# Performance work log

Hardware: AMD Instinct MI355X
Metric: run time of the kernel (lower is better)

Reference implementation:

```python
import jax, jax.numpy as jnp
import numpy as np

B, S, H = 4, 256, 768
NUM_BASIC = 4
NUM_REL = 32            # labels 1..31 are real edges, 0 = no edge
NUM_ALL = 2 * NUM_REL   # bidir: forward slots 0..31, reverse slots 33..63


def setup_inputs() -> dict:
    key = jax.random.key(0)
    k1, k2, k3, k4, k5 = jax.random.split(key, 5)
    hidden_states = jax.random.normal(k1, (B, S, H), dtype=jnp.float32)
    rels = jax.random.randint(k2, (B, S, S), 0, NUM_REL, dtype=jnp.int32)
    # xavier-ish init scale for params
    basic_matrix = jax.random.normal(k3, (NUM_BASIC, H, H), dtype=jnp.float32) * 0.02
    rel_weight = jax.random.normal(k4, (NUM_ALL, NUM_BASIC), dtype=jnp.float32) * 0.1
    self_weight = jax.random.normal(k5, (H, H), dtype=jnp.float32) * 0.02  # Linear weight (out,in)
    return {"hidden_states": hidden_states, "rels": rels,
            "basic_matrix": basic_matrix, "rel_weight": rel_weight,
            "self_weight": self_weight}


def reference(hidden_states, rels, basic_matrix, rel_weight, self_weight):
    dt = hidden_states.dtype
    # forward-direction one-hot relation tensor [B, NUM_ALL, S, S], masked where rels == 0
    fwd_mask = (rels > 0).astype(dt)                                   # [B,S,S]
    fwd_oh = jax.nn.one_hot(rels, NUM_ALL, axis=1, dtype=dt) * fwd_mask[:, None]
    # reverse direction (bidir): labels shifted by NUM_REL, zeroed where no edge
    rev_rels_raw = jnp.transpose(rels, (0, 2, 1))
    rev_rels = jnp.where(rev_rels_raw > 0, rev_rels_raw + NUM_REL, 0)  # {0} U {33..63}
    rev_mask = (rev_rels > 0).astype(dt)
    rev_oh = jax.nn.one_hot(rev_rels, NUM_ALL, axis=1, dtype=dt) * rev_mask[:, None]
    rel_tensor = fwd_oh + rev_oh                                       # [B,R,S,S]

    # basis decomposition: per-relation transform [R, H, H]
    rel_matrix = jnp.einsum('rb,bio->rio', rel_weight, basic_matrix)
    # per-relation transformed hidden states [B,R,S,H]
    r_hidden = jnp.einsum('bsi,rio->brso', hidden_states, rel_matrix)
    # adjacency aggregation [B,R,S,H]
    r_ctx = jnp.einsum('brij,brjo->brio', rel_tensor, r_hidden)
    # mean over neighbors (clamp count at 1)
    num_neighbors = jnp.maximum(rel_tensor.sum(-1), 1.0)               # [B,R,S]
    r_ctx = r_ctx / num_neighbors[..., None]
    context = r_ctx.sum(axis=1)                                        # [B,S,H]
    self_layer = hidden_states @ self_weight.T
    return self_layer + context
```

## Files before the change

### kernel.cpp

```cpp
#include <hip/hip_runtime.h>
#include <stdint.h>

typedef unsigned short u16;
typedef unsigned int u32;
typedef __attribute__((ext_vector_type(8))) short short8;
typedef __attribute__((ext_vector_type(4))) float float4v;

#define Bb 4
#define Ss 256
#define Hh 768
#define NALL 64


__device__ __forceinline__ float b2f(u16 h) {
    u32 u = ((u32)h) << 16;
    float f;
    __builtin_memcpy(&f, &u, 4);
    return f;
}
__device__ __forceinline__ u16 f2b(float f) {
    u32 u;
    __builtin_memcpy(&u, &f, 4);
    u = (u + 0x7fffu + ((u >> 16) & 1u)) >> 16;
    return (u16)u;
}
union pk8 { uint4 v; u16 e[8]; };
__device__ __forceinline__ uint4 cvt8(float4 f0, float4 f1) {
    pk8 r;
    r.e[0] = f2b(f0.x); r.e[1] = f2b(f0.y); r.e[2] = f2b(f0.z); r.e[3] = f2b(f0.w);
    r.e[4] = f2b(f1.x); r.e[5] = f2b(f1.y); r.e[6] = f2b(f1.z); r.e[7] = f2b(f1.w);
    return r.v;
}

__device__ __forceinline__ void gemm_tile(const float* __restrict__ aB,
                                          const float* __restrict__ bB,
                                          int niter, u16* As, u16* Bs,
                                          float4v* acc, int t) {
    const int row = t >> 2, kk = (t & 3) * 16;
    const int w = t >> 6, l = t & 63, quad = l >> 4, l16 = l & 15;
#pragma unroll
    for (int c = 0; c < 4; ++c) acc[c] = (float4v){0.f, 0.f, 0.f, 0.f};
    float4 a0 = *(const float4*)aB, a1 = *(const float4*)(aB + 4);
    float4 a2 = *(const float4*)(aB + 8), a3 = *(const float4*)(aB + 12);
    float4 b0 = *(const float4*)bB, b1 = *(const float4*)(bB + 4);
    float4 b2 = *(const float4*)(bB + 8), b3 = *(const float4*)(bB + 12);
    for (int s = 0; s < niter; ++s) {
        __syncthreads();
        *(uint4*)(&As[row * 72 + kk]) = cvt8(a0, a1);
        *(uint4*)(&As[row * 72 + kk + 8]) = cvt8(a2, a3);
        *(uint4*)(&Bs[row * 72 + kk]) = cvt8(b0, b1);
        *(uint4*)(&Bs[row * 72 + kk + 8]) = cvt8(b2, b3);
        __syncthreads();
        if (s + 1 < niter) {
            const float* ap = aB + (s + 1) * 64;
            const float* bp = bB + (s + 1) * 64;
            a0 = *(const float4*)ap; a1 = *(const float4*)(ap + 4);
            a2 = *(const float4*)(ap + 8); a3 = *(const float4*)(ap + 12);
            b0 = *(const float4*)bp; b1 = *(const float4*)(bp + 4);
            b2 = *(const float4*)(bp + 8); b3 = *(const float4*)(bp + 12);
        }
#pragma unroll
        for (int k2 = 0; k2 < 64; k2 += 32) {
            const short8 af = *(const short8*)(&As[(16 * w + l16) * 72 + k2 + quad * 8]);
#pragma unroll
            for (int c = 0; c < 4; ++c) {
                const short8 bfr = *(const short8*)(&Bs[(16 * c + l16) * 72 + k2 + quad * 8]);
                acc[c] = __builtin_amdgcn_mfma_f32_16x16x32_bf16(af, bfr, acc[c], 0, 0, 0);
            }
        }
    }
}

__global__ __launch_bounds__(256, 4) void k_phase1(const float* __restrict__ h,
                                                   const int* __restrict__ rels,
                                                   const float* __restrict__ basic,
                                                   const float* __restrict__ relw,
                                                   const float* __restrict__ selfw,
                                                   u16* __restrict__ coefC,
                                                   u16* __restrict__ Gt,
                                                   u16* __restrict__ S) {
    __shared__ __align__(16) u16 As[64 * 72];
    __shared__ __align__(16) u16 Bs[64 * 72];
    const int t = threadIdx.x;
    const int z = blockIdx.x;
    const int row = t >> 2, kk = (t & 3) * 16;
    const int w = t >> 6, l = t & 63, quad = l >> 4, l16 = l & 15;

    if (z < 768) {
        const int ot = z % 12, jt = (z / 12) % 4, bk = z / 48;
        const int b = bk >> 2, q = bk & 3;
        const float* aB = h + ((size_t)b * Ss + jt * 64 + row) * Hh + kk;
        const float* bp = basic + ((size_t)q * Hh + row) * Hh + ot * 64 + kk;

        float4v acc[4];
#pragma unroll
        for (int c = 0; c < 4; ++c) acc[c] = (float4v){0.f, 0.f, 0.f, 0.f};
        float4 a0 = *(const float4*)aB, a1 = *(const float4*)(aB + 4);
        float4 a2 = *(const float4*)(aB + 8), a3 = *(const float4*)(aB + 12);
        float4 b0 = *(const float4*)bp, b1 = *(const float4*)(bp + 4);
        float4 b2 = *(const float4*)(bp + 8), b3 = *(const float4*)(bp + 12);

        for (int s = 0; s < 12; ++s) {
            __syncthreads();
            *(uint4*)(&As[row * 72 + kk]) = cvt8(a0, a1);
            *(uint4*)(&As[row * 72 + kk + 8]) = cvt8(a2, a3);
            {
                pk8 t0, t1;
                t0.v = cvt8(b0, b1);
                t1.v = cvt8(b2, b3);
#pragma unroll
                for (int m = 0; m < 8; ++m) Bs[(kk + m) * 72 + row] = t0.e[m];
#pragma unroll
                for (int m = 0; m < 8; ++m) Bs[(kk + 8 + m) * 72 + row] = t1.e[m];
            }
            __syncthreads();
            if (s + 1 < 12) {
                const float* ap = aB + (s + 1) * 64;
                const float* bq = bp + (size_t)(s + 1) * 64 * Hh;
                a0 = *(const float4*)ap; a1 = *(const float4*)(ap + 4);
                a2 = *(const float4*)(ap + 8); a3 = *(const float4*)(ap + 12);
                b0 = *(const float4*)bq; b1 = *(const float4*)(bq + 4);
                b2 = *(const float4*)(bq + 8); b3 = *(const float4*)(bq + 12);
            }
#pragma unroll
            for (int k2 = 0; k2 < 64; k2 += 32) {
                const short8 af = *(const short8*)(&As[(16 * w + l16) * 72 + k2 + quad * 8]);
#pragma unroll
                for (int c = 0; c < 4; ++c) {
                    const short8 bfr = *(const short8*)(&Bs[(16 * c + l16) * 72 + k2 + quad * 8]);
                    acc[c] = __builtin_amdgcn_mfma_f32_16x16x32_bf16(af, bfr, acc[c], 0, 0, 0);
                }
            }
        }
        __syncthreads();
#pragma unroll
        for (int c = 0; c < 4; ++c)
#pragma unroll
            for (int r = 0; r < 4; ++r)
                As[(16 * c + l16) * 72 + 16 * w + quad * 4 + r] = f2b(acc[c][r]);
        __syncthreads();
#pragma unroll
        for (int uu = 0; uu < 2; ++uu) {
            const int u = t + uu * 256;
            const int oo = u >> 3, ch = u & 7;
            *(uint4*)(&Gt[((size_t)bk * Hh + ot * 64 + oo) * Ss + jt * 64 + ch * 8]) =
                *(const uint4*)(&As[oo * 72 + ch * 8]);
        }
    } else if (z < 960) {
        const int u = z - 768;
        const int ot = u % 12, it = (u / 12) % 4, b = u / 48;
        const float* aB = h + ((size_t)b * Ss + it * 64 + row) * Hh + kk;
        const float* bB = selfw + (size_t)(ot * 64 + row) * Hh + kk;
        float4v acc[4];
        gemm_tile(aB, bB, 12, As, Bs, acc, t);
#pragma unroll
        for (int c = 0; c < 4; ++c)
#pragma unroll
            for (int r = 0; r < 4; ++r) {
                const int il = 16 * w + quad * 4 + r;
                const int ol = 16 * c + l16;
                S[((size_t)b * Ss + it * 64 + il) * Hh + ot * 64 + ol] = f2b(acc[c][r]);
            }
    } else {
        float* srelw = (float*)As;
        u32* hist = (u32*)Bs;
        const int r = z - 960;
        const int i = r & 255, b = r >> 8;
        srelw[t] = relw[t];
        if (t < NALL) hist[t] = 0u;
        __syncthreads();
        const int rfw = rels[(b * Ss + i) * Ss + t];
        const int rcl = rels[(b * Ss + t) * Ss + i];
        if (rfw > 0) atomicAdd(&hist[rfw], 1u);
        if (rcl > 0) atomicAdd(&hist[rcl + 32], 1u);
        __syncthreads();
        float c0 = 0.f, c1 = 0.f, c2 = 0.f, c3 = 0.f;
        if (rfw > 0) {
            const float inv = 1.0f / (float)hist[rfw];
            c0 += srelw[rfw * 4 + 0] * inv; c1 += srelw[rfw * 4 + 1] * inv;
            c2 += srelw[rfw * 4 + 2] * inv; c3 += srelw[rfw * 4 + 3] * inv;
        }
        if (rcl > 0) {
            const int rr = rcl + 32;
            const float inv = 1.0f / (float)hist[rr];
            c0 += srelw[rr * 4 + 0] * inv; c1 += srelw[rr * 4 + 1] * inv;
            c2 += srelw[rr * 4 + 2] * inv; c3 += srelw[rr * 4 + 3] * inv;
        }
        const size_t base = ((size_t)(b * 4) * Ss + i) * Ss + t;
        coefC[base] = f2b(c0);
        coefC[base + (size_t)Ss * Ss] = f2b(c1);
        coefC[base + (size_t)2 * Ss * Ss] = f2b(c2);
        coefC[base + (size_t)3 * Ss * Ss] = f2b(c3);
    }
}

__global__ __launch_bounds__(256, 4) void k_phase2(const u16* __restrict__ coefC,
                                                   const u16* __restrict__ Gt,
                                                   const u16* __restrict__ S,
                                                   float* __restrict__ out) {
    __shared__ __align__(16) u16 As[64 * 72];
    __shared__ __align__(16) u16 Bs[64 * 72];
    const int z = blockIdx.x;
    const int ot = z % 12, it = (z / 12) % 4, b = z / 48;
    const int t = threadIdx.x;
    const int row = t >> 2, kk = (t & 3) * 16;
    const int w = t >> 6, l = t & 63, quad = l >> 4, l16 = l & 15;

    auto aa = [&](int s) -> const u16* {
        return coefC + ((size_t)(b * 4 + (s >> 2)) * Ss + it * 64 + row) * Ss + (s & 3) * 64 + kk;
    };
    auto bb = [&](int s) -> const u16* {
        return Gt + ((size_t)(b * 4 + (s >> 2)) * Hh + ot * 64 + row) * Ss + (s & 3) * 64 + kk;
    };

    float4v acc[4];
#pragma unroll
    for (int c = 0; c < 4; ++c) acc[c] = (float4v){0.f, 0.f, 0.f, 0.f};
    uint4 a0 = *(const uint4*)aa(0);
    uint4 a1 = *(const uint4*)(aa(0) + 8);
    uint4 b0 = *(const uint4*)bb(0);
    uint4 b1 = *(const uint4*)(bb(0) + 8);

    for (int s = 0; s < 16; ++s) {
        __syncthreads();
        *(uint4*)(&As[row * 72 + kk]) = a0;
        *(uint4*)(&As[row * 72 + kk + 8]) = a1;
        *(uint4*)(&Bs[row * 72 + kk]) = b0;
        *(uint4*)(&Bs[row * 72 + kk + 8]) = b1;
        __syncthreads();
        if (s + 1 < 16) {
            const u16* ap = aa(s + 1);
            const u16* bp = bb(s + 1);
            a0 = *(const uint4*)ap;
            a1 = *(const uint4*)(ap + 8);
            b0 = *(const uint4*)bp;
            b1 = *(const uint4*)(bp + 8);
        }
#pragma unroll
        for (int k2 = 0; k2 < 64; k2 += 32) {
            const short8 af = *(const short8*)(&As[(16 * w + l16) * 72 + k2 + quad * 8]);
#pragma unroll
            for (int c = 0; c < 4; ++c) {
                const short8 bfr = *(const short8*)(&Bs[(16 * c + l16) * 72 + k2 + quad * 8]);
                acc[c] = __builtin_amdgcn_mfma_f32_16x16x32_bf16(af, bfr, acc[c], 0, 0, 0);
            }
        }
    }

#pragma unroll
    for (int c = 0; c < 4; ++c)
#pragma unroll
        for (int r = 0; r < 4; ++r) {
            const int il = 16 * w + quad * 4 + r;
            const int ol = 16 * c + l16;
            const size_t idx = ((size_t)b * Ss + it * 64 + il) * Hh + ot * 64 + ol;
            out[idx] = acc[c][r] + b2f(S[idx]);
        }
}

extern "C" void kernel_launch(void* const* d_in, const int* in_sizes, int n_in,
                              void* d_out, int out_size, void* d_ws, size_t ws_size,
                              hipStream_t stream) {
    const float* h = (const float*)d_in[0];
    const int* rels = (const int*)d_in[1];
    const float* basic = (const float*)d_in[2];
    const float* relw = (const float*)d_in[3];
    const float* selfw = (const float*)d_in[4];
    float* out = (float*)d_out;

    u16* coefC = (u16*)d_ws;
    u16* Gt = coefC + (size_t)Bb * 4 * Ss * Ss;
    u16* S = Gt + (size_t)Bb * 4 * Hh * Ss;

    k_phase1<<<1984, 256, 0, stream>>>(h, rels, basic, relw, selfw, coefC, Gt, S);
    k_phase2<<<192, 256, 0, stream>>>(coefC, Gt, S, out);
}
```

Before: 108.3 us.

## Pre-convert inputs to bf16, add transposed basis, fuse self-linear into aggregation GEMM

Adds a prep kernel that converts hidden states, self weight and a transposed copy of the basis matrices to bf16 up front and computes the coefficient matrix. A separate kernel then computes Gt from bf16 operands with vectorized loads, dropping the strided scalar LDS transpose and the per-tile fp32 conversions. The self-linear GEMM is folded into the phase-2 K loop as 12 extra iterations, so the bf16 S intermediate and its readback go away. In exchange there are three launches instead of two, extra global round trips for the converted copies, and a longer serial K loop in phase 2 running on only 192 blocks.

```diff
diff --git a/kernel.cpp b/kernel.cpp
--- a/kernel.cpp
+++ b/kernel.cpp
@@ -24,147 +24,36 @@
     u = (u + 0x7fffu + ((u >> 16) & 1u)) >> 16;
     return (u16)u;
 }
-union pk8 { uint4 v; u16 e[8]; };
-__device__ __forceinline__ uint4 cvt8(float4 f0, float4 f1) {
-    pk8 r;
-    r.e[0] = f2b(f0.x); r.e[1] = f2b(f0.y); r.e[2] = f2b(f0.z); r.e[3] = f2b(f0.w);
-    r.e[4] = f2b(f1.x); r.e[5] = f2b(f1.y); r.e[6] = f2b(f1.z); r.e[7] = f2b(f1.w);
-    return r.v;
-}
-
-__device__ __forceinline__ void gemm_tile(const float* __restrict__ aB,
-                                          const float* __restrict__ bB,
-                                          int niter, u16* As, u16* Bs,
-                                          float4v* acc, int t) {
-    const int row = t >> 2, kk = (t & 3) * 16;
-    const int w = t >> 6, l = t & 63, quad = l >> 4, l16 = l & 15;
-#pragma unroll
-    for (int c = 0; c < 4; ++c) acc[c] = (float4v){0.f, 0.f, 0.f, 0.f};
-    float4 a0 = *(const float4*)aB, a1 = *(const float4*)(aB + 4);
-    float4 a2 = *(const float4*)(aB + 8), a3 = *(const float4*)(aB + 12);
-    float4 b0 = *(const float4*)bB, b1 = *(const float4*)(bB + 4);
-    float4 b2 = *(const float4*)(bB + 8), b3 = *(const float4*)(bB + 12);
-    for (int s = 0; s < niter; ++s) {
-        __syncthreads();
-        *(uint4*)(&As[row * 72 + kk]) = cvt8(a0, a1);
-        *(uint4*)(&As[row * 72 + kk + 8]) = cvt8(a2, a3);
-        *(uint4*)(&Bs[row * 72 + kk]) = cvt8(b0, b1);
-        *(uint4*)(&Bs[row * 72 + kk + 8]) = cvt8(b2, b3);
-        __syncthreads();
-        if (s + 1 < niter) {
-            const float* ap = aB + (s + 1) * 64;
-            const float* bp = bB + (s + 1) * 64;
-            a0 = *(const float4*)ap; a1 = *(const float4*)(ap + 4);
-            a2 = *(const float4*)(ap + 8); a3 = *(const float4*)(ap + 12);
-            b0 = *(const float4*)bp; b1 = *(const float4*)(bp + 4);
-            b2 = *(const float4*)(bp + 8); b3 = *(const float4*)(bp + 12);
-        }
-#pragma unroll
-        for (int k2 = 0; k2 < 64; k2 += 32) {
-            const short8 af = *(const short8*)(&As[(16 * w + l16) * 72 + k2 + quad * 8]);
-#pragma unroll
-            for (int c = 0; c < 4; ++c) {
-                const short8 bfr = *(const short8*)(&Bs[(16 * c + l16) * 72 + k2 + quad * 8]);
-                acc[c] = __builtin_amdgcn_mfma_f32_16x16x32_bf16(af, bfr, acc[c], 0, 0, 0);
-            }
-        }
-    }
-}
-
-__global__ __launch_bounds__(256, 4) void k_phase1(const float* __restrict__ h,
-                                                   const int* __restrict__ rels,
-                                                   const float* __restrict__ basic,
-                                                   const float* __restrict__ relw,
-                                                   const float* __restrict__ selfw,
-                                                   u16* __restrict__ coefC,
-                                                   u16* __restrict__ Gt,
-                                                   u16* __restrict__ S) {
-    __shared__ __align__(16) u16 As[64 * 72];
-    __shared__ __align__(16) u16 Bs[64 * 72];
+
+__global__ __launch_bounds__(256) void k_prep(const float* __restrict__ h,
+                                              const int* __restrict__ rels,
+                                              const float* __restrict__ basic,
+                                              const float* __restrict__ relw,
+                                              const float* __restrict__ selfw,
+                                              u16* __restrict__ basicT,
+                                              u16* __restrict__ coefC,
+                                              u16* __restrict__ hbf,
+                                              u16* __restrict__ swbf) {
+    __shared__ u16 tile[32][34];
+    __shared__ float srelw[256];
+    __shared__ u32 hist[NALL];
+    const int z = blockIdx.x;
     const int t = threadIdx.x;
-    const int z = blockIdx.x;
-    const int row = t >> 2, kk = (t & 3) * 16;
-    const int w = t >> 6, l = t & 63, quad = l >> 4, l16 = l & 15;
-
-    if (z < 768) {
-        const int ot = z % 12, jt = (z / 12) % 4, bk = z / 48;
-        const int b = bk >> 2, q = bk & 3;
-        const float* aB = h + ((size_t)b * Ss + jt * 64 + row) * Hh + kk;
-        const float* bp = basic + ((size_t)q * Hh + row) * Hh + ot * 64 + kk;
-
-        float4v acc[4];
-#pragma unroll
-        for (int c = 0; c < 4; ++c) acc[c] = (float4v){0.f, 0.f, 0.f, 0.f};
-        float4 a0 = *(const float4*)aB, a1 = *(const float4*)(aB + 4);
-        float4 a2 = *(const float4*)(aB + 8), a3 = *(const float4*)(aB + 12);
-        float4 b0 = *(const float4*)bp, b1 = *(const float4*)(bp + 4);
-        float4 b2 = *(const float4*)(bp + 8), b3 = *(const float4*)(bp + 12);
-
-        for (int s = 0; s < 12; ++s) {
-            __syncthreads();
-            *(uint4*)(&As[row * 72 + kk]) = cvt8(a0, a1);
-            *(uint4*)(&As[row * 72 + kk + 8]) = cvt8(a2, a3);
-            {
-                pk8 t0, t1;
-                t0.v = cvt8(b0, b1);
-                t1.v = cvt8(b2, b3);
-#pragma unroll
-                for (int m = 0; m < 8; ++m) Bs[(kk + m) * 72 + row] = t0.e[m];
-#pragma unroll
-                for (int m = 0; m < 8; ++m) Bs[(kk + 8 + m) * 72 + row] = t1.e[m];
-            }
-            __syncthreads();
-            if (s + 1 < 12) {
-                const float* ap = aB + (s + 1) * 64;
-                const float* bq = bp + (size_t)(s + 1) * 64 * Hh;
-                a0 = *(const float4*)ap; a1 = *(const float4*)(ap + 4);
-                a2 = *(const float4*)(ap + 8); a3 = *(const float4*)(ap + 12);
-                b0 = *(const float4*)bq; b1 = *(const float4*)(bq + 4);
-                b2 = *(const float4*)(bq + 8); b3 = *(const float4*)(bq + 12);
-            }
-#pragma unroll
-            for (int k2 = 0; k2 < 64; k2 += 32) {
-                const short8 af = *(const short8*)(&As[(16 * w + l16) * 72 + k2 + quad * 8]);
-#pragma unroll
-                for (int c = 0; c < 4; ++c) {
-                    const short8 bfr = *(const short8*)(&Bs[(16 * c + l16) * 72 + k2 + quad * 8]);
-                    acc[c] = __builtin_amdgcn_mfma_f32_16x16x32_bf16(af, bfr, acc[c], 0, 0, 0);
-                }
-            }
-        }
-        __syncthreads();
-#pragma unroll
-        for (int c = 0; c < 4; ++c)
-#pragma unroll
-            for (int r = 0; r < 4; ++r)
-                As[(16 * c + l16) * 72 + 16 * w + quad * 4 + r] = f2b(acc[c][r]);
-        __syncthreads();
-#pragma unroll
-        for (int uu = 0; uu < 2; ++uu) {
-            const int u = t + uu * 256;
-            const int oo = u >> 3, ch = u & 7;
-            *(uint4*)(&Gt[((size_t)bk * Hh + ot * 64 + oo) * Ss + jt * 64 + ch * 8]) =
-                *(const uint4*)(&As[oo * 72 + ch * 8]);
-        }
-    } else if (z < 960) {
-        const int u = z - 768;
-        const int ot = u % 12, it = (u / 12) % 4, b = u / 48;
-        const float* aB = h + ((size_t)b * Ss + it * 64 + row) * Hh + kk;
-        const float* bB = selfw + (size_t)(ot * 64 + row) * Hh + kk;
-        float4v acc[4];
-        gemm_tile(aB, bB, 12, As, Bs, acc, t);
-#pragma unroll
-        for (int c = 0; c < 4; ++c)
-#pragma unroll
-            for (int r = 0; r < 4; ++r) {
-                const int il = 16 * w + quad * 4 + r;
-                const int ol = 16 * c + l16;
-                S[((size_t)b * Ss + it * 64 + il) * Hh + ot * 64 + ol] = f2b(acc[c][r]);
-            }
-    } else {
-        float* srelw = (float*)As;
-        u32* hist = (u32*)Bs;
-        const int r = z - 960;
+
+    if (z < 2304) {
+        const int q = z / 576, rem = z % 576;
+        const int i0 = (rem % 24) * 32, o0 = (rem / 24) * 32;
+        const int tx = t & 31, ty = t >> 5;
+        const size_t base = (size_t)q * Hh * Hh;
+#pragma unroll
+        for (int r = 0; r < 4; ++r)
+            tile[ty + 8 * r][tx] = f2b(basic[base + (size_t)(i0 + ty + 8 * r) * Hh + o0 + tx]);
+        __syncthreads();
+#pragma unroll
+        for (int r = 0; r < 4; ++r)
+            basicT[base + (size_t)(o0 + ty + 8 * r) * Hh + i0 + tx] = tile[tx][ty + 8 * r];
+    } else if (z < 3328) {
+        const int r = z - 2304;
         const int i = r & 255, b = r >> 8;
         srelw[t] = relw[t];
         if (t < NALL) hist[t] = 0u;
@@ -191,12 +80,80 @@
         coefC[base + (size_t)Ss * Ss] = f2b(c1);
         coefC[base + (size_t)2 * Ss * Ss] = f2b(c2);
         coefC[base + (size_t)3 * Ss * Ss] = f2b(c3);
+    } else if (z < 4096) {
+        const size_t i = ((size_t)(z - 3328) * 256 + t) * 4;
+        const float4 v = *(const float4*)(h + i);
+        u32 lo = (u32)f2b(v.x) | ((u32)f2b(v.y) << 16);
+        u32 hi = (u32)f2b(v.z) | ((u32)f2b(v.w) << 16);
+        *(uint2*)(hbf + i) = make_uint2(lo, hi);
+    } else {
+        const size_t i = ((size_t)(z - 4096) * 256 + t) * 4;
+        const float4 v = *(const float4*)(selfw + i);
+        u32 lo = (u32)f2b(v.x) | ((u32)f2b(v.y) << 16);
+        u32 hi = (u32)f2b(v.z) | ((u32)f2b(v.w) << 16);
+        *(uint2*)(swbf + i) = make_uint2(lo, hi);
     }
+}
+
+__global__ __launch_bounds__(256, 4) void k_mid(const u16* __restrict__ basicT,
+                                                const u16* __restrict__ hbf,
+                                                u16* __restrict__ Gt) {
+    __shared__ __align__(16) u16 As[64 * 72];
+    __shared__ __align__(16) u16 Bs[64 * 72];
+    const int z = blockIdx.x;
+    const int o0 = (z % 12) * 64, j0 = ((z / 12) % 4) * 64, bk = z / 48;
+    const int b = bk >> 2, q = bk & 3;
+    const int t = threadIdx.x;
+    const int row = t >> 2, kk = (t & 3) * 16;
+    const int w = t >> 6, l = t & 63, quad = l >> 4, l16 = l & 15;
+
+    const u16* aB = basicT + ((size_t)q * Hh + o0 + row) * Hh + kk;
+    const u16* bB = hbf + ((size_t)b * Ss + j0 + row) * Hh + kk;
+
+    float4v acc[4];
+#pragma unroll
+    for (int c = 0; c < 4; ++c) acc[c] = (float4v){0.f, 0.f, 0.f, 0.f};
+    uint4 a0 = *(const uint4*)aB, a1 = *(const uint4*)(aB + 8);
+    uint4 b0 = *(const uint4*)bB, b1 = *(const uint4*)(bB + 8);
+
+    for (int s = 0; s < 12; ++s) {
+        __syncthreads();
+        *(uint4*)(&As[row * 72 + kk]) = a0;
+        *(uint4*)(&As[row * 72 + kk + 8]) = a1;
+        *(uint4*)(&Bs[row * 72 + kk]) = b0;
+        *(uint4*)(&Bs[row * 72 + kk + 8]) = b1;
+        __syncthreads();
+        if (s + 1 < 12) {
+            a0 = *(const uint4*)(aB + (s + 1) * 64);
+            a1 = *(const uint4*)(aB + (s + 1) * 64 + 8);
+            b0 = *(const uint4*)(bB + (s + 1) * 64);
+            b1 = *(const uint4*)(bB + (s + 1) * 64 + 8);
+        }
+#pragma unroll
+        for (int k2 = 0; k2 < 64; k2 += 32) {
+            const short8 af = *(const short8*)(&As[(16 * w + l16) * 72 + k2 + quad * 8]);
+#pragma unroll
+            for (int c = 0; c < 4; ++c) {
+                const short8 bfr = *(const short8*)(&Bs[(16 * c + l16) * 72 + k2 + quad * 8]);
+                acc[c] = __builtin_amdgcn_mfma_f32_16x16x32_bf16(af, bfr, acc[c], 0, 0, 0);
+            }
+        }
+    }
+
+#pragma unroll
+    for (int c = 0; c < 4; ++c)
+#pragma unroll
+        for (int r = 0; r < 4; ++r) {
+            const int ol = 16 * w + quad * 4 + r;
+            const int jl = 16 * c + l16;
+            Gt[((size_t)bk * Hh + o0 + ol) * Ss + j0 + jl] = f2b(acc[c][r]);
+        }
 }
 
 __global__ __launch_bounds__(256, 4) void k_phase2(const u16* __restrict__ coefC,
                                                    const u16* __restrict__ Gt,
-                                                   const u16* __restrict__ S,
+                                                   const u16* __restrict__ hbf,
+                                                   const u16* __restrict__ swbf,
                                                    float* __restrict__ out) {
     __shared__ __align__(16) u16 As[64 * 72];
     __shared__ __align__(16) u16 Bs[64 * 72];
@@ -207,10 +164,14 @@
     const int w = t >> 6, l = t & 63, quad = l >> 4, l16 = l & 15;
 
     auto aa = [&](int s) -> const u16* {
-        return coefC + ((size_t)(b * 4 + (s >> 2)) * Ss + it * 64 + row) * Ss + (s & 3) * 64 + kk;
+        if (s < 16)
+            return coefC + ((size_t)(b * 4 + (s >> 2)) * Ss + it * 64 + row) * Ss + (s & 3) * 64 + kk;
+        return hbf + ((size_t)b * Ss + it * 64 + row) * Hh + (s - 16) * 64 + kk;
     };
     auto bb = [&](int s) -> const u16* {
-        return Gt + ((size_t)(b * 4 + (s >> 2)) * Hh + ot * 64 + row) * Ss + (s & 3) * 64 + kk;
+        if (s < 16)
+            return Gt + ((size_t)(b * 4 + (s >> 2)) * Hh + ot * 64 + row) * Ss + (s & 3) * 64 + kk;
+        return swbf + (size_t)(ot * 64 + row) * Hh + (s - 16) * 64 + kk;
     };
 
     float4v acc[4];
@@ -221,14 +182,14 @@
     uint4 b0 = *(const uint4*)bb(0);
     uint4 b1 = *(const uint4*)(bb(0) + 8);
 
-    for (int s = 0; s < 16; ++s) {
+    for (int s = 0; s < 28; ++s) {
         __syncthreads();
         *(uint4*)(&As[row * 72 + kk]) = a0;
         *(uint4*)(&As[row * 72 + kk + 8]) = a1;
         *(uint4*)(&Bs[row * 72 + kk]) = b0;
         *(uint4*)(&Bs[row * 72 + kk + 8]) = b1;
         __syncthreads();
-        if (s + 1 < 16) {
+        if (s + 1 < 28) {
             const u16* ap = aa(s + 1);
             const u16* bp = bb(s + 1);
             a0 = *(const uint4*)ap;
@@ -253,8 +214,7 @@
         for (int r = 0; r < 4; ++r) {
             const int il = 16 * w + quad * 4 + r;
             const int ol = 16 * c + l16;
-            const size_t idx = ((size_t)b * Ss + it * 64 + il) * Hh + ot * 64 + ol;
-            out[idx] = acc[c][r] + b2f(S[idx]);
+            out[((size_t)b * Ss + it * 64 + il) * Hh + ot * 64 + ol] = acc[c][r];
         }
 }
 
@@ -268,10 +228,13 @@
     const float* selfw = (const float*)d_in[4];
     float* out = (float*)d_out;
 
-    u16* coefC = (u16*)d_ws;
+    u16* basicT = (u16*)d_ws;
+    u16* coefC = basicT + (size_t)4 * Hh * Hh;
     u16* Gt = coefC + (size_t)Bb * 4 * Ss * Ss;
-    u16* S = Gt + (size_t)Bb * 4 * Hh * Ss;
-
-    k_phase1<<<1984, 256, 0, stream>>>(h, rels, basic, relw, selfw, coefC, Gt, S);
-    k_phase2<<<192, 256, 0, stream>>>(coefC, Gt, S, out);
-}
+    u16* hbf = Gt + (size_t)Bb * 4 * Hh * Ss;
+    u16* swbf = hbf + (size_t)Bb * Ss * Hh;
+
+    k_prep<<<4672, 256, 0, stream>>>(h, rels, basic, relw, selfw, basicT, coefC, hbf, swbf);
+    k_mid<<<768, 256, 0, stream>>>(basicT, hbf, Gt);
+    k_phase2<<<192, 256, 0, stream>>>(coefC, Gt, hbf, swbf, out);
+}
```

Result: faster. 104.2 us (-3.8%).
